# Kernel tuning notes

Measured on AMD Instinct MI355X. Metric: run time of the kernel, lower is better.

The kernel has to match this reference:

```python
import jax, jax.numpy as jnp
import numpy as np

IGNORE_INDEX = -100  # torch default; targets here are all valid but mask is honored
REDUCTION = "mean"

B, D, V = 4096, 2048, 32000


def setup_inputs() -> dict:
    key = jax.random.key(0)
    k1, k2, k3 = jax.random.split(key, 3)
    x = jax.random.normal(k1, (B, D), dtype=jnp.float32)
    # LM-head weight, scaled like typical init
    L = jax.random.normal(k2, (V, D), dtype=jnp.float32) * (1.0 / np.sqrt(D))
    target = jax.random.randint(k3, (B,), 0, V, dtype=jnp.int64)
    class_weight = jnp.ones((V,), dtype=jnp.float32)  # unnormalized per-class weight
    return {"x": x, "L": L, "target": target, "class_weight": class_weight}


def reference(x, L, target, class_weight):
    """Fused linear + weighted cross-entropy (reduction='mean', ignore_index=-100).

    Equivalent math to MyLinearCrossEntropyFunction: the torch code chunks over
    batches/classes/features with an online softmax solely to avoid materializing
    logits; the unchunked math is a single GEMM + stable log-softmax CE.
    """
    # logits: [B, V]
    logits = jnp.einsum("bd,vd->bv", x, L)
    logZ = jax.nn.logsumexp(logits, axis=1)                      # [B]
    valid = target != IGNORE_INDEX                               # [B] bool
    t_safe = jnp.where(valid, target, 0)
    gathered = jnp.take_along_axis(logits, t_safe[:, None], axis=1)[:, 0]  # [B]
    # effective per-sample weight: class weight of target, zeroed where ignored
    wt = jnp.where(valid, class_weight[t_safe], jnp.zeros((), logits.dtype))  # [B]
    per_sample = wt * (logZ - gathered)
    total = per_sample.sum()
    if REDUCTION == "mean":
        return total / wt.sum()
    return total
```

## Files before the change

kernel.cpp:

```cpp
#include <hip/hip_runtime.h>

#define B_ 4096
#define D_ 2048
#define V_ 32000

#define BM 256
#define BN 256
#define BKB 128
#define NT (D_ / BKB)
#define NCHUNK (V_ / 64)

typedef __attribute__((ext_vector_type(8))) int   int8v;
typedef __attribute__((ext_vector_type(4))) int   int4v;
typedef __attribute__((ext_vector_type(4))) float f32x4;

#define SCALE_A 127
#define SCALE_B 121

__device__ __forceinline__ void load_lds16(const void* g, void* l) {
    __builtin_amdgcn_global_load_lds(
        (const __attribute__((address_space(1))) void*)g,
        (__attribute__((address_space(3))) void*)l,
        16, 0, 0);
}

__global__ void cast_f32_to_fp8(const float* __restrict__ x,
                                const float* __restrict__ L,
                                unsigned int* __restrict__ xq,
                                unsigned int* __restrict__ Lq) {
    const int n4x = (B_ * D_) / 4;
    const int n4l = (V_ * D_) / 4;
    int i = blockIdx.x * blockDim.x + threadIdx.x;
    const float* in; unsigned int* out; float ps; int j;
    if (i < n4x) { in = x; out = xq; ps = 1.0f;  j = i; }
    else         { j = i - n4x; if (j >= n4l) return; in = L; out = Lq; ps = 64.0f; }
    float4 v = ((const float4*)in)[j];
    int w = __builtin_amdgcn_cvt_pk_fp8_f32(v.x * ps, v.y * ps, 0, false);
    w     = __builtin_amdgcn_cvt_pk_fp8_f32(v.z * ps, v.w * ps, w, true);
    out[j] = (unsigned)w;
}

__global__ __launch_bounds__(512, 2)
void gemm_ce_partials(const unsigned char* __restrict__ xq,
                      const unsigned char* __restrict__ Lq,
                      const int* __restrict__ targ,
                      float2* __restrict__ partials,
                      float* __restrict__ gathered) {
    __shared__ __align__(16) unsigned char As[2][BM * BKB];
    __shared__ __align__(16) unsigned char Bs[2][BN * BKB];

    const int tid    = threadIdx.x;
    const int lane   = tid & 63;
    const int wid    = tid >> 6;
    const int wave_m = wid >> 2;
    const int wave_n = wid & 3;
    const int quad   = lane >> 4;
    const int l16    = lane & 15;
    const int swz    = l16 & 7;

    const int m0 = blockIdx.x * BM;
    const int n0 = blockIdx.y * BN;

    const unsigned char* srcA[4];
    const unsigned char* srcB[4];
    int dstoff[4];
#pragma unroll
    for (int p = 0; p < 4; ++p) {
        int flat = p * 512 + tid;
        int row  = flat >> 3;
        int pc   = flat & 7;
        int c    = pc ^ (row & 7);
        dstoff[p] = flat * 16;
        srcA[p] = xq + (size_t)(m0 + row) * D_ + c * 16;
        srcB[p] = Lq + (size_t)(n0 + row) * D_ + c * 16;
    }

    f32x4 acc[8][4];
#pragma unroll
    for (int i = 0; i < 8; ++i)
#pragma unroll
        for (int j = 0; j < 4; ++j)
            acc[i][j] = (f32x4){0.f, 0.f, 0.f, 0.f};

    const int p0 = ((quad ^ swz) << 4);
    const int p1 = p0 ^ 64;

#pragma unroll
    for (int p = 0; p < 4; ++p) {
        load_lds16(srcA[p], &As[0][dstoff[p]]);
        load_lds16(srcB[p], &Bs[0][dstoff[p]]);
    }
    asm volatile("s_waitcnt vmcnt(0)" ::: "memory");
    __builtin_amdgcn_s_barrier();

    for (int kt = 0; kt < NT; ++kt) {
        const int cur = kt & 1;
        const int nxt = cur ^ 1;
        const int k1  = (kt + 1) * BKB;
        const bool pf = (kt + 1 < NT);

        int8v a[4], b[4];

#pragma unroll
        for (int mi = 0; mi < 4; ++mi) {
            int base = (wave_m * 128 + mi * 16 + l16) * BKB;
            union { int8v v8; int4v v4[2]; } u;
            u.v4[0] = *(const int4v*)&As[cur][base + p0];
            u.v4[1] = *(const int4v*)&As[cur][base + p1];
            a[mi] = u.v8;
        }
#pragma unroll
        for (int ni = 0; ni < 2; ++ni) {
            int base = (wave_n * 64 + ni * 16 + l16) * BKB;
            union { int8v v8; int4v v4[2]; } u;
            u.v4[0] = *(const int4v*)&Bs[cur][base + p0];
            u.v4[1] = *(const int4v*)&Bs[cur][base + p1];
            b[ni] = u.v8;
        }
        if (pf) {
#pragma unroll
            for (int p = 0; p < 4; ++p)
                load_lds16(srcA[p] + k1, &As[nxt][dstoff[p]]);
        }
        __builtin_amdgcn_s_barrier();
        __builtin_amdgcn_s_setprio(1);
#pragma unroll
        for (int mi = 0; mi < 4; ++mi)
#pragma unroll
            for (int ni = 0; ni < 2; ++ni)
                acc[mi][ni] = __builtin_amdgcn_mfma_scale_f32_16x16x128_f8f6f4(
                    a[mi], b[ni], acc[mi][ni], 0, 0, 0, SCALE_A, 0, SCALE_B);
        __builtin_amdgcn_s_setprio(0);
        __builtin_amdgcn_s_barrier();

#pragma unroll
        for (int ni = 2; ni < 4; ++ni) {
            int base = (wave_n * 64 + ni * 16 + l16) * BKB;
            union { int8v v8; int4v v4[2]; } u;
            u.v4[0] = *(const int4v*)&Bs[cur][base + p0];
            u.v4[1] = *(const int4v*)&Bs[cur][base + p1];
            b[ni] = u.v8;
        }
        if (pf) {
#pragma unroll
            for (int p = 0; p < 4; ++p)
                load_lds16(srcB[p] + k1, &Bs[nxt][dstoff[p]]);
        }
        __builtin_amdgcn_s_barrier();
        __builtin_amdgcn_s_setprio(1);
#pragma unroll
        for (int mi = 0; mi < 4; ++mi)
#pragma unroll
            for (int ni = 2; ni < 4; ++ni)
                acc[mi][ni] = __builtin_amdgcn_mfma_scale_f32_16x16x128_f8f6f4(
                    a[mi], b[ni], acc[mi][ni], 0, 0, 0, SCALE_A, 0, SCALE_B);
        __builtin_amdgcn_s_setprio(0);
        __builtin_amdgcn_s_barrier();

#pragma unroll
        for (int mi = 0; mi < 4; ++mi) {
            int base = (wave_m * 128 + (mi + 4) * 16 + l16) * BKB;
            union { int8v v8; int4v v4[2]; } u;
            u.v4[0] = *(const int4v*)&As[cur][base + p0];
            u.v4[1] = *(const int4v*)&As[cur][base + p1];
            a[mi] = u.v8;
        }
        __builtin_amdgcn_s_barrier();
        __builtin_amdgcn_s_setprio(1);
#pragma unroll
        for (int mi = 0; mi < 4; ++mi)
#pragma unroll
            for (int ni = 0; ni < 2; ++ni)
                acc[mi + 4][ni] = __builtin_amdgcn_mfma_scale_f32_16x16x128_f8f6f4(
                    a[mi], b[ni], acc[mi + 4][ni], 0, 0, 0, SCALE_A, 0, SCALE_B);
        __builtin_amdgcn_s_setprio(0);
        __builtin_amdgcn_s_barrier();

        __builtin_amdgcn_s_setprio(1);
#pragma unroll
        for (int mi = 0; mi < 4; ++mi)
#pragma unroll
            for (int ni = 2; ni < 4; ++ni)
                acc[mi + 4][ni] = __builtin_amdgcn_mfma_scale_f32_16x16x128_f8f6f4(
                    a[mi], b[ni], acc[mi + 4][ni], 0, 0, 0, SCALE_A, 0, SCALE_B);
        __builtin_amdgcn_s_setprio(0);
        asm volatile("s_waitcnt vmcnt(0)" ::: "memory");
        __builtin_amdgcn_s_barrier();
    }

    const int row_base = m0 + wave_m * 128;
    const int col_base = n0 + wave_n * 64;
    const int chunk    = blockIdx.y * 4 + wave_n;

    int tv[32];
#pragma unroll
    for (int mi = 0; mi < 8; ++mi)
#pragma unroll
        for (int r = 0; r < 4; ++r)
            tv[mi * 4 + r] = targ[row_base + mi * 16 + quad * 4 + r];

    float M = acc[0][0][0];
#pragma unroll
    for (int mi = 0; mi < 8; ++mi)
#pragma unroll
        for (int ni = 0; ni < 4; ++ni)
#pragma unroll
            for (int r = 0; r < 4; ++r)
                M = fmaxf(M, acc[mi][ni][r]);
#pragma unroll
    for (int off = 1; off < 64; off <<= 1)
        M = fmaxf(M, __shfl_xor(M, off, 64));

    float sv[32];
#pragma unroll
    for (int mi = 0; mi < 8; ++mi)
#pragma unroll
        for (int r = 0; r < 4; ++r)
            sv[mi * 4 + r] = __expf(acc[mi][0][r] - M) + __expf(acc[mi][1][r] - M) +
                             __expf(acc[mi][2][r] - M) + __expf(acc[mi][3][r] - M);
#pragma unroll
    for (int off = 1; off < 16; off <<= 1)
#pragma unroll
        for (int i = 0; i < 32; ++i)
            sv[i] += __shfl_xor(sv[i], off, 64);

    if (l16 == 0) {
#pragma unroll
        for (int mi = 0; mi < 8; ++mi)
#pragma unroll
            for (int r = 0; r < 4; ++r) {
                int row = row_base + mi * 16 + quad * 4 + r;
                partials[(size_t)row * NCHUNK + chunk] = make_float2(M, sv[mi * 4 + r]);
            }
    }

#pragma unroll
    for (int mi = 0; mi < 8; ++mi)
#pragma unroll
        for (int r = 0; r < 4; ++r) {
            int row = row_base + mi * 16 + quad * 4 + r;
            int cb  = col_base + l16;
            int t   = tv[mi * 4 + r];
            if (cb      == t) gathered[row] = acc[mi][0][r];
            if (cb + 16 == t) gathered[row] = acc[mi][1][r];
            if (cb + 32 == t) gathered[row] = acc[mi][2][r];
            if (cb + 48 == t) gathered[row] = acc[mi][3][r];
        }
}

__global__ void combine_rows(const float2* __restrict__ partials,
                             const float* __restrict__ gathered,
                             const int* __restrict__ targ,
                             const float* __restrict__ cw,
                             float* __restrict__ row_loss,
                             float* __restrict__ row_w) {
    int row  = blockIdx.x * 4 + (threadIdx.x >> 6);
    int lane = threadIdx.x & 63;
    float m = -3.0e38f, s = 0.f;
    for (int c = lane; c < NCHUNK; c += 64) {
        float2 p = partials[(size_t)row * NCHUNK + c];
        float nm = fmaxf(m, p.x);
        s = s * __expf(m - nm) + p.y * __expf(p.x - nm);
        m = nm;
    }
#pragma unroll
    for (int off = 32; off; off >>= 1) {
        float om = __shfl_xor(m, off, 64);
        float os = __shfl_xor(s, off, 64);
        float nm = fmaxf(m, om);
        s = s * __expf(m - nm) + os * __expf(om - nm);
        m = nm;
    }
    if (lane == 0) {
        float logZ = m + __logf(s);
        int t = targ[row];
        bool valid = (t != -100);
        int ts = valid ? t : 0;
        float w = valid ? cw[ts] : 0.f;
        row_loss[row] = w * (logZ - gathered[row]);
        row_w[row]    = w;
    }
}

__global__ void final_reduce(const float* __restrict__ rl,
                             const float* __restrict__ rw,
                             float* __restrict__ out) {
    __shared__ float sl[4], sw[4];
    float a = 0.f, b = 0.f;
    for (int i = threadIdx.x; i < B_; i += 256) { a += rl[i]; b += rw[i]; }
#pragma unroll
    for (int off = 32; off; off >>= 1) {
        a += __shfl_xor(a, off, 64);
        b += __shfl_xor(b, off, 64);
    }
    int w = threadIdx.x >> 6;
    if ((threadIdx.x & 63) == 0) { sl[w] = a; sw[w] = b; }
    __syncthreads();
    if (threadIdx.x == 0) {
        float ta = sl[0] + sl[1] + sl[2] + sl[3];
        float tb = sw[0] + sw[1] + sw[2] + sw[3];
        out[0] = ta / tb;
    }
}

extern "C" void kernel_launch(void* const* d_in, const int* in_sizes, int n_in,
                              void* d_out, int out_size, void* d_ws, size_t ws_size,
                              hipStream_t stream) {
    const float* x  = (const float*)d_in[0];
    const float* L  = (const float*)d_in[1];
    const int* targ = (const int*)d_in[2];
    const float* cw = (const float*)d_in[3];
    float* out = (float*)d_out;

    char* ws = (char*)d_ws;
    size_t o = 0;
    unsigned char* xq = (unsigned char*)(ws + o);  o += (size_t)B_ * D_;
    unsigned char* Lq = (unsigned char*)(ws + o);  o += (size_t)V_ * D_;
    float2* partials = (float2*)(ws + o);          o += (size_t)B_ * NCHUNK * 8;
    float* gathered = (float*)(ws + o);            o += (size_t)B_ * 4;
    float* row_loss = (float*)(ws + o);            o += (size_t)B_ * 4;
    float* row_w    = (float*)(ws + o);            o += (size_t)B_ * 4;
    (void)ws_size;

    {
        int n4 = (B_ * D_) / 4 + (V_ * D_) / 4;
        cast_f32_to_fp8<<<(n4 + 255) / 256, 256, 0, stream>>>(
            x, L, (unsigned*)xq, (unsigned*)Lq);
    }

    {
        dim3 grid(B_ / BM, V_ / BN);
        gemm_ce_partials<<<grid, 512, 0, stream>>>(xq, Lq, targ, partials, gathered);
    }

    combine_rows<<<B_ / 4, 256, 0, stream>>>(partials, gathered, targ, cw, row_loss, row_w);

    final_reduce<<<1, 256, 0, stream>>>(row_loss, row_w, out);
}
```

Measured before the change: 658.7 us.

## Reschedule FP8 GEMM main loop with interleaved fragment loads and fewer barriers

Restructures the k-loop of the fused FP8 GEMM plus cross-entropy kernel. The old version ran four phases, each fenced by two barriers. The new one uses four phases with one barrier each. LDS fragment reads, global-to-LDS prefetch of the next tile, and MFMA groups are interleaved so later fragments load while earlier MFMAs can issue, and the same fragment registers are reused across rows. Prefetch addressing is simplified to one base pointer per operand plus constant strides, which saves address registers. The gain depends on whether the compiler keeps this schedule. MFMA groups are now uneven in size, and the reduced synchronization could expose LDS latency.

Result: no change. 650.2 us (-1.3%).

```diff
diff --git a/kernel.cpp b/kernel.cpp
--- a/kernel.cpp
+++ b/kernel.cpp
@@ -22,6 +22,13 @@
         (const __attribute__((address_space(1))) void*)g,
         (__attribute__((address_space(3))) void*)l,
         16, 0, 0);
+}
+
+__device__ __forceinline__ int8v frag(const unsigned char* buf, int base, int p0, int p1) {
+    union { int8v v8; int4v v4[2]; } u;
+    u.v4[0] = *(const int4v*)(buf + base + p0);
+    u.v4[1] = *(const int4v*)(buf + base + p1);
+    return u.v8;
 }
 
 __global__ void cast_f32_to_fp8(const float* __restrict__ x,
@@ -61,19 +68,13 @@
     const int m0 = blockIdx.x * BM;
     const int n0 = blockIdx.y * BN;
 
-    const unsigned char* srcA[4];
-    const unsigned char* srcB[4];
-    int dstoff[4];
-#pragma unroll
-    for (int p = 0; p < 4; ++p) {
-        int flat = p * 512 + tid;
-        int row  = flat >> 3;
-        int pc   = flat & 7;
-        int c    = pc ^ (row & 7);
-        dstoff[p] = flat * 16;
-        srcA[p] = xq + (size_t)(m0 + row) * D_ + c * 16;
-        srcB[p] = Lq + (size_t)(n0 + row) * D_ + c * 16;
-    }
+    const int r0 = tid >> 3;
+    const int c0 = (tid & 7) ^ (r0 & 7);
+    const unsigned char* sA = xq + (size_t)(m0 + r0) * D_ + c0 * 16;
+    const unsigned char* sB = Lq + (size_t)(n0 + r0) * D_ + c0 * 16;
+    const int d0 = tid * 16;
+#define STEP (64 * D_)
+#define DSTEP 8192
 
     f32x4 acc[8][4];
 #pragma unroll
@@ -85,10 +86,18 @@
     const int p0 = ((quad ^ swz) << 4);
     const int p1 = p0 ^ 64;
 
+    const int arow = (wave_m * 128 + l16) * BKB;
+    const int brow = (wave_n * 64 + l16) * BKB;
+#define AB(mi) (arow + (mi) * (16 * BKB))
+#define BB(ni) (brow + (ni) * (16 * BKB))
+#define MM(A, B, MI, NI)                                                     \
+    acc[MI][NI] = __builtin_amdgcn_mfma_scale_f32_16x16x128_f8f6f4(          \
+        A, B, acc[MI][NI], 0, 0, 0, SCALE_A, 0, SCALE_B)
+
 #pragma unroll
     for (int p = 0; p < 4; ++p) {
-        load_lds16(srcA[p], &As[0][dstoff[p]]);
-        load_lds16(srcB[p], &Bs[0][dstoff[p]]);
+        load_lds16(sA + (size_t)p * STEP, &As[0][d0 + p * DSTEP]);
+        load_lds16(sB + (size_t)p * STEP, &Bs[0][d0 + p * DSTEP]);
     }
     asm volatile("s_waitcnt vmcnt(0)" ::: "memory");
     __builtin_amdgcn_s_barrier();
@@ -96,93 +105,64 @@
     for (int kt = 0; kt < NT; ++kt) {
         const int cur = kt & 1;
         const int nxt = cur ^ 1;
-        const int k1  = (kt + 1) * BKB;
+        const size_t k1 = (size_t)(kt + 1) * BKB;
         const bool pf = (kt + 1 < NT);
-
-        int8v a[4], b[4];
-
-#pragma unroll
-        for (int mi = 0; mi < 4; ++mi) {
-            int base = (wave_m * 128 + mi * 16 + l16) * BKB;
-            union { int8v v8; int4v v4[2]; } u;
-            u.v4[0] = *(const int4v*)&As[cur][base + p0];
-            u.v4[1] = *(const int4v*)&As[cur][base + p1];
-            a[mi] = u.v8;
-        }
-#pragma unroll
-        for (int ni = 0; ni < 2; ++ni) {
-            int base = (wave_n * 64 + ni * 16 + l16) * BKB;
-            union { int8v v8; int4v v4[2]; } u;
-            u.v4[0] = *(const int4v*)&Bs[cur][base + p0];
-            u.v4[1] = *(const int4v*)&Bs[cur][base + p1];
-            b[ni] = u.v8;
-        }
+        const unsigned char* Ac = As[cur];
+        const unsigned char* Bc = Bs[cur];
+
+        int8v a0, a1, a2, a3, b0, b1, b2, b3, s;
+
+        a0 = frag(Ac, AB(0), p0, p1);
+        a1 = frag(Ac, AB(1), p0, p1);
+        b0 = frag(Bc, BB(0), p0, p1);
+        a2 = frag(Ac, AB(2), p0, p1);
+        a3 = frag(Ac, AB(3), p0, p1);
+        b1 = frag(Bc, BB(1), p0, p1);
         if (pf) {
-#pragma unroll
-            for (int p = 0; p < 4; ++p)
-                load_lds16(srcA[p] + k1, &As[nxt][dstoff[p]]);
+            load_lds16(sB + k1, &Bs[nxt][d0]);
+            load_lds16(sB + k1 + (size_t)STEP, &Bs[nxt][d0 + DSTEP]);
         }
         __builtin_amdgcn_s_barrier();
         __builtin_amdgcn_s_setprio(1);
-#pragma unroll
-        for (int mi = 0; mi < 4; ++mi)
-#pragma unroll
-            for (int ni = 0; ni < 2; ++ni)
-                acc[mi][ni] = __builtin_amdgcn_mfma_scale_f32_16x16x128_f8f6f4(
-                    a[mi], b[ni], acc[mi][ni], 0, 0, 0, SCALE_A, 0, SCALE_B);
+        MM(a0, b0, 0, 0); MM(a1, b0, 1, 0);
         __builtin_amdgcn_s_setprio(0);
-        __builtin_amdgcn_s_barrier();
-
-#pragma unroll
-        for (int ni = 2; ni < 4; ++ni) {
-            int base = (wave_n * 64 + ni * 16 + l16) * BKB;
-            union { int8v v8; int4v v4[2]; } u;
-            u.v4[0] = *(const int4v*)&Bs[cur][base + p0];
-            u.v4[1] = *(const int4v*)&Bs[cur][base + p1];
-            b[ni] = u.v8;
-        }
+
+        b2 = frag(Bc, BB(2), p0, p1);
+        b3 = frag(Bc, BB(3), p0, p1);
+        s  = frag(Ac, AB(4), p0, p1);
         if (pf) {
-#pragma unroll
-            for (int p = 0; p < 4; ++p)
-                load_lds16(srcB[p] + k1, &Bs[nxt][dstoff[p]]);
+            load_lds16(sB + k1 + (size_t)2 * STEP, &Bs[nxt][d0 + 2 * DSTEP]);
+            load_lds16(sB + k1 + (size_t)3 * STEP, &Bs[nxt][d0 + 3 * DSTEP]);
         }
         __builtin_amdgcn_s_barrier();
         __builtin_amdgcn_s_setprio(1);
-#pragma unroll
-        for (int mi = 0; mi < 4; ++mi)
-#pragma unroll
-            for (int ni = 2; ni < 4; ++ni)
-                acc[mi][ni] = __builtin_amdgcn_mfma_scale_f32_16x16x128_f8f6f4(
-                    a[mi], b[ni], acc[mi][ni], 0, 0, 0, SCALE_A, 0, SCALE_B);
+        MM(a2, b0, 2, 0); MM(a3, b0, 3, 0);
+        MM(a0, b1, 0, 1); MM(a1, b1, 1, 1); MM(a2, b1, 2, 1); MM(a3, b1, 3, 1);
         __builtin_amdgcn_s_setprio(0);
-        __builtin_amdgcn_s_barrier();
-
-#pragma unroll
-        for (int mi = 0; mi < 4; ++mi) {
-            int base = (wave_m * 128 + (mi + 4) * 16 + l16) * BKB;
-            union { int8v v8; int4v v4[2]; } u;
-            u.v4[0] = *(const int4v*)&As[cur][base + p0];
-            u.v4[1] = *(const int4v*)&As[cur][base + p1];
-            a[mi] = u.v8;
+
+        if (pf) {
+            load_lds16(sA + k1, &As[nxt][d0]);
+            load_lds16(sA + k1 + (size_t)STEP, &As[nxt][d0 + DSTEP]);
         }
         __builtin_amdgcn_s_barrier();
         __builtin_amdgcn_s_setprio(1);
-#pragma unroll
-        for (int mi = 0; mi < 4; ++mi)
-#pragma unroll
-            for (int ni = 0; ni < 2; ++ni)
-                acc[mi + 4][ni] = __builtin_amdgcn_mfma_scale_f32_16x16x128_f8f6f4(
-                    a[mi], b[ni], acc[mi + 4][ni], 0, 0, 0, SCALE_A, 0, SCALE_B);
+        MM(a0, b2, 0, 2); MM(a1, b2, 1, 2); MM(a2, b2, 2, 2); MM(a3, b2, 3, 2);
+        MM(a0, b3, 0, 3); MM(a1, b3, 1, 3); MM(a2, b3, 2, 3); MM(a3, b3, 3, 3);
         __builtin_amdgcn_s_setprio(0);
-        __builtin_amdgcn_s_barrier();
-
+
+        a0 = frag(Ac, AB(5), p0, p1);
+        a1 = frag(Ac, AB(6), p0, p1);
+        a2 = frag(Ac, AB(7), p0, p1);
+        if (pf) {
+            load_lds16(sA + k1 + (size_t)2 * STEP, &As[nxt][d0 + 2 * DSTEP]);
+            load_lds16(sA + k1 + (size_t)3 * STEP, &As[nxt][d0 + 3 * DSTEP]);
+        }
+        __builtin_amdgcn_s_barrier();
         __builtin_amdgcn_s_setprio(1);
-#pragma unroll
-        for (int mi = 0; mi < 4; ++mi)
-#pragma unroll
-            for (int ni = 2; ni < 4; ++ni)
-                acc[mi + 4][ni] = __builtin_amdgcn_mfma_scale_f32_16x16x128_f8f6f4(
-                    a[mi], b[ni], acc[mi + 4][ni], 0, 0, 0, SCALE_A, 0, SCALE_B);
+        MM(s, b0, 4, 0); MM(s, b1, 4, 1); MM(s, b2, 4, 2); MM(s, b3, 4, 3);
+        MM(a0, b0, 5, 0); MM(a0, b1, 5, 1); MM(a0, b2, 5, 2); MM(a0, b3, 5, 3);
+        MM(a1, b0, 6, 0); MM(a1, b1, 6, 1); MM(a1, b2, 6, 2); MM(a1, b3, 6, 3);
+        MM(a2, b0, 7, 0); MM(a2, b1, 7, 1); MM(a2, b2, 7, 2); MM(a2, b3, 7, 3);
         __builtin_amdgcn_s_setprio(0);
         asm volatile("s_waitcnt vmcnt(0)" ::: "memory");
         __builtin_amdgcn_s_barrier();
```
